# Performance work log

Measured on AMD Instinct MI355X. Metric: run time of the kernel, lower is better.

The kernel has to match this reference:

```python
import jax, jax.numpy as jnp
import numpy as np


def _build_space_group(L):
    # C4v point group: rotations R^k and mirror*R^k, acting on Z_L^2 coords.
    R = np.array([[0, -1], [1, 0]])
    Mr = np.array([[1, 0], [0, -1]])
    mats = [np.linalg.matrix_power(R, k) for k in range(4)]
    mats += [Mr @ m for m in mats[:4]]
    mats = np.array(mats)  # (8,2,2)
    P = 8

    def find(A):
        for i in range(P):
            if np.array_equal(mats[i], A):
                return i
        raise ValueError('point group not closed')

    pcomp = np.array([[find(mats[a] @ mats[b]) for b in range(P)] for a in range(P)])
    pinv = np.array([find(np.round(np.linalg.inv(mats[a])).astype(int)) for a in range(P)])

    N = L * L
    G = P * N
    gx, gy = np.meshgrid(np.arange(L), np.arange(L), indexing='ij')
    coords = np.stack([gx.ravel(), gy.ravel()], -1)  # (N,2): site coords, also translation vecs

    # element g = p*N + (tx*L+ty) acts on coord v as  M_p v + t  (mod L)
    perms = np.zeros((G, N), np.int64)
    for p in range(P):
        w = coords @ mats[p].T  # (N,2)
        for t in range(N):
            u = (w + coords[t]) % L
            perms[p * N + t] = u[:, 0] * L + u[:, 1]

    pa = np.repeat(np.arange(P), N)  # point part per element
    ta = np.tile(coords, (P, 1))     # translation part per element
    mult = np.zeros((G, G), np.int64)
    for g in range(G):
        Ma = mats[pa[g]]
        pprod = pcomp[pa[g], pa]            # (G,)
        tprod = (ta @ Ma.T + ta[g]) % L     # (G,2): M_a t_b + t_a
        mult[g] = pprod * N + tprod[:, 0] * L + tprod[:, 1]
    inv = np.zeros((G,), np.int64)
    for g in range(G):
        Mi = mats[pinv[pa[g]]]
        ti = (-(Mi @ ta[g])) % L            # -M^{-1} t
        inv[g] = pinv[pa[g]] * N + ti[0] * L + ti[1]
    return perms, mult, inv


L_SIDE = 8
FEATS = (8, 8, 8)
BATCH = 1024


def setup_inputs() -> dict:
    perms, mult, inv = _build_space_group(L_SIDE)
    N = L_SIDE * L_SIDE
    G = perms.shape[0]
    c0, c1, c2 = FEATS
    ks = jax.random.split(jax.random.key(0), 8)
    s = jax.random.normal(ks[0], (BATCH, N), jnp.float32)
    # lecun_normal: std = 1/sqrt(fan_in)
    W_lift = jax.random.normal(ks[1], (N, c0), jnp.float32) / np.sqrt(N)
    b_lift = jnp.zeros((c0,), jnp.float32)
    K0 = jax.random.normal(ks[2], (G, c0, c1), jnp.float32) / np.sqrt(G * c0)
    K1 = jax.random.normal(ks[3], (G, c1, c2), jnp.float32) / np.sqrt(G * c1)
    W_amp = jax.random.normal(ks[4], (c2, 1), jnp.float32) / np.sqrt(c2)
    b_amp = jnp.zeros((1,), jnp.float32)
    W_ph = jnp.zeros((c2, 1), jnp.float32)  # zeros init as in module
    b_ph = jnp.zeros((1,), jnp.float32)
    return {'s': s, 'perms': jnp.asarray(perms), 'mult': jnp.asarray(mult),
            'inv': jnp.asarray(inv), 'W_lift': W_lift, 'b_lift': b_lift,
            'K0': K0, 'K1': K1, 'W_amp': W_amp, 'b_amp': b_amp,
            'W_ph': W_ph, 'b_ph': b_ph}


def reference(s, perms, mult, inv, W_lift, b_lift, K0, K1, W_amp, b_amp, W_ph, b_ph):
    G = perms.shape[0]
    s_g = s[:, perms].astype(jnp.float32)          # (B,G,N): lift gather
    x = jax.nn.gelu(s_g @ W_lift + b_lift)         # (B,G,c0)
    T = mult[:, inv]                                # (G,G): T[g,h] = g * h^{-1}
    scale = 1.0 / jnp.sqrt(jnp.asarray(G, jnp.float32))
    for K in (K0, K1):
        Kg = K[T]                                   # (G,G,cin,cout) regular-rep kernel gather
        x = jax.nn.gelu(jnp.einsum('bhc,ghcd->bgd', x, Kg) * scale)
    pooled = jnp.mean(x, axis=1)                    # trivial irrep: chi = 1/G
    amp = (pooled @ W_amp + b_amp)[..., 0]          # (B,)
    phase = (pooled @ W_ph + b_ph)[..., 0]
    return (amp + 1j * phase).astype(jnp.complex64)
```

## Files before the change

kernel.cpp:

```cpp
#include <hip/hip_runtime.h>
#include <hip/hip_bf16.h>
#include <cstdint>
#include <cstddef>

using s16x8 = __attribute__((ext_vector_type(8))) short;
using u16x8 = __attribute__((ext_vector_type(8))) unsigned short;
using f32x4 = __attribute__((ext_vector_type(4))) float;

#define GC 4096
#define SCALE_G 0.04419417382415922f

__device__ __forceinline__ float gelu_f(float x) {
  float u = 0.7978845608028654f * (x + 0.044715f * x * x * x);
  return 0.5f * x * (1.0f + tanhf(u));
}

__device__ __forceinline__ unsigned short f2bf(float f) {
  unsigned int u = __float_as_uint(f);
  unsigned int r = (u + 0x7fffu + ((u >> 16) & 1u)) >> 16;
  return (unsigned short)r;
}
__device__ __forceinline__ float bf2f(unsigned short b) {
  return __uint_as_float(((unsigned int)b) << 16);
}

__device__ __forceinline__ int idx_stride(const int* __restrict__ identity_row) {
  return (identity_row[1] == 0 && identity_row[3] == 0 && identity_row[5] == 0) ? 2 : 1;
}

typedef __attribute__((address_space(1))) void gvoid;
typedef __attribute__((address_space(3))) void lvoid;
__device__ __forceinline__ void gld16(const void* g, void* l) {
  __builtin_amdgcn_global_load_lds((gvoid*)g, (lvoid*)l, 16, 0, 0);
}

__device__ __forceinline__ s16x8 gload16(const unsigned short* p) {
  s16x8 r;
  asm volatile("global_load_dwordx4 %0, %1, off" : "=v"(r) : "v"(p));
  return r;
}

__global__ __launch_bounds__(256) void k_prep(
    const float* __restrict__ s, const int* __restrict__ perms,
    const int* __restrict__ mult, const int* __restrict__ inv,
    const float* __restrict__ Wl, const float* __restrict__ K0,
    const float* __restrict__ K1,
    unsigned short* __restrict__ sb, unsigned short* __restrict__ WPT,
    unsigned int* __restrict__ TallP, unsigned short* __restrict__ K0T0,
    unsigned short* __restrict__ K0T1) {
  const int tid = blockIdx.x * 256 + threadIdx.x;
  if (tid < 65536) {
    sb[tid] = f2bf(s[tid]);
  } else if (tid < 98304) {
    const int st = idx_stride(perms);
    const int t2 = tid - 65536;
    const int n = t2 & 63, h = t2 >> 6;
    const int m = perms[(size_t)t2 * st];
#pragma unroll
    for (int c = 0; c < 8; ++c)
      WPT[(size_t)((h << 3) + c) * 64 + m] = f2bf(Wl[n * 8 + c]);
  } else if (tid < 229376) {
    const int st = idx_stride(mult);
    const int i3 = tid - 98304;
    const int g = i3 & 511, w = i3 >> 9;
    const int h0 = (w >> 2) * 8 + (w & 3), h1 = h0 + 4;
    const int ih0 = inv[(size_t)h0 * st], ih1 = inv[(size_t)h1 * st];
    const unsigned int tv0 = (unsigned int)mult[(size_t)((g << 9) + ih0) * st];
    const unsigned int tv1 = (unsigned int)mult[(size_t)((g << 9) + ih1) * st];
    TallP[(size_t)w * 512 + g] = tv0 | (tv1 << 16);
  } else if (tid < 262144) {
    const int t4 = tid - 229376;
    const int tgh = t4 >> 6, e = t4 & 63, d = e >> 3, c = e & 7;
    K0T0[tgh * 64 + d * 8 + c] = f2bf(K0[tgh * 64 + c * 8 + d]);
  } else if (tid < 294912) {
    const int t5 = tid - 262144;
    const int tgh = t5 >> 6, e = t5 & 63, d = e >> 3, c = e & 7;
    K0T1[tgh * 64 + d * 8 + c] = f2bf(K1[tgh * 64 + c * 8 + d]);
  }
}

__global__ __launch_bounds__(256) void gemm_bf16(
    const unsigned short* __restrict__ A,
    const unsigned short* __restrict__ BT,
    unsigned short* __restrict__ C,
    const float* __restrict__ bias8,
    float scale, int M, int N, int K) {
  constexpr int BM = 64, BN = 128, BK = 64;
  __shared__ __align__(16) unsigned short As[3][BM * BK];
  __shared__ __align__(16) unsigned short Bs[3][BN * BK];

  const int nbm = M / BM;
  int bid = blockIdx.x;
  {
    const int q = (nbm * (N / BN)) >> 3;
    bid = (bid & 7) * q + (bid >> 3);
  }
  const int bn = bid / nbm, bm = bid % nbm;

  const int t = threadIdx.x;
  const int wid = t >> 6, lane = t & 63;
  const int wm = (wid >> 1) << 5;
  const int wn = (wid & 1) << 6;
  const int lr = lane & 15, lq = lane >> 4;

  const unsigned short* gA[2];
  const unsigned short* gB[4];
#pragma unroll
  for (int is = 0; is < 2; ++is) {
    const int sidx = is * 256 + t, row = sidx >> 3, c = (sidx & 7) ^ (row & 7);
    gA[is] = A + (size_t)(bm * BM + row) * K + c * 8;
  }
#pragma unroll
  for (int is = 0; is < 4; ++is) {
    const int sidx = is * 256 + t, row = sidx >> 3, c = (sidx & 7) ^ (row & 7);
    gB[is] = BT + (size_t)(bn * BN + row) * K + c * 8;
  }

  int aoff[2][2], boff[4][2];
#pragma unroll
  for (int i = 0; i < 2; ++i) {
    const int row = wm + i * 16 + lr;
#pragma unroll
    for (int ks = 0; ks < 2; ++ks)
      aoff[i][ks] = (row * 8 + ((ks * 4 + lq) ^ (row & 7))) * 16;
  }
#pragma unroll
  for (int j = 0; j < 4; ++j) {
    const int row = wn + j * 16 + lr;
#pragma unroll
    for (int ks = 0; ks < 2; ++ks)
      boff[j][ks] = (row * 8 + ((ks * 4 + lq) ^ (row & 7))) * 16;
  }

  auto stage = [&](int kt, int buf) {
    const int koff = kt * BK;
    char* la = (char*)&As[buf][0];
    char* lb = (char*)&Bs[buf][0];
#pragma unroll
    for (int is = 0; is < 2; ++is) gld16(gA[is] + koff, la + (is * 256 + t) * 16);
#pragma unroll
    for (int is = 0; is < 4; ++is) gld16(gB[is] + koff, lb + (is * 256 + t) * 16);
  };

  f32x4 acc[2][4] = {};
  const int nt = K / BK;
  stage(0, 0);
  if (nt > 1) stage(1, 1);

  int cur = 0;
  for (int kt = 0; kt < nt; ++kt) {
    if (kt < nt - 1) asm volatile("s_waitcnt vmcnt(6)" ::: "memory");
    else             asm volatile("s_waitcnt vmcnt(0)" ::: "memory");
    __builtin_amdgcn_s_barrier();
    asm volatile("" ::: "memory");
    __builtin_amdgcn_sched_barrier(0);
    if (kt + 2 < nt) {
      int nb = cur + 2; if (nb >= 3) nb -= 3;
      stage(kt + 2, nb);
    }
    const char* Ac = (const char*)&As[cur][0];
    const char* Bc = (const char*)&Bs[cur][0];
#pragma unroll
    for (int ks = 0; ks < 2; ++ks) {
      s16x8 a0 = *(const s16x8*)(Ac + aoff[0][ks]);
      s16x8 a1 = *(const s16x8*)(Ac + aoff[1][ks]);
      s16x8 b0 = *(const s16x8*)(Bc + boff[0][ks]);
      s16x8 b1 = *(const s16x8*)(Bc + boff[1][ks]);
      s16x8 b2 = *(const s16x8*)(Bc + boff[2][ks]);
      s16x8 b3 = *(const s16x8*)(Bc + boff[3][ks]);
      acc[0][0] = __builtin_amdgcn_mfma_f32_16x16x32_bf16(a0, b0, acc[0][0], 0, 0, 0);
      acc[0][1] = __builtin_amdgcn_mfma_f32_16x16x32_bf16(a0, b1, acc[0][1], 0, 0, 0);
      acc[0][2] = __builtin_amdgcn_mfma_f32_16x16x32_bf16(a0, b2, acc[0][2], 0, 0, 0);
      acc[0][3] = __builtin_amdgcn_mfma_f32_16x16x32_bf16(a0, b3, acc[0][3], 0, 0, 0);
      acc[1][0] = __builtin_amdgcn_mfma_f32_16x16x32_bf16(a1, b0, acc[1][0], 0, 0, 0);
      acc[1][1] = __builtin_amdgcn_mfma_f32_16x16x32_bf16(a1, b1, acc[1][1], 0, 0, 0);
      acc[1][2] = __builtin_amdgcn_mfma_f32_16x16x32_bf16(a1, b2, acc[1][2], 0, 0, 0);
      acc[1][3] = __builtin_amdgcn_mfma_f32_16x16x32_bf16(a1, b3, acc[1][3], 0, 0, 0);
    }
    cur = (cur == 2) ? 0 : cur + 1;
  }

#pragma unroll
  for (int i = 0; i < 2; ++i) {
    const int row0 = bm * BM + wm + i * 16 + lq * 4;
#pragma unroll
    for (int j = 0; j < 4; ++j) {
      const int col = bn * BN + wn + j * 16 + lr;
      const float bv = bias8 ? bias8[col & 7] : 0.0f;
#pragma unroll
      for (int r = 0; r < 4; ++r) {
        float v = gelu_f(acc[i][j][r] * scale + bv);
        C[(size_t)(row0 + r) * N + col] = f2bf(v);
      }
    }
  }
}

template <int POOL>
__global__ __launch_bounds__(512, 2) void gemm_fused(
    const unsigned short* __restrict__ A,
    const unsigned short* __restrict__ K0T,
    const unsigned int* __restrict__ TallP,
    unsigned short* __restrict__ C,
    float* __restrict__ Ppart,
    float scale) {
  constexpr int Kdim = 4096, N = 4096, BM = 128, BK = 64, NT = Kdim / BK;
  __shared__ __align__(16) unsigned short As[3][BM * BK];
  __shared__ __align__(16) unsigned int TlP[64 * 4 * 16];

  const int bm = blockIdx.x & 7;
  const int bn = blockIdx.x >> 3;

  const int t = threadIdx.x;
  const int wid = t >> 6, lane = t & 63;
  const int wm = (wid >> 2) << 6;
  const int wn = (wid & 3) << 5;
  const int lr = lane & 15, lq = lane >> 4;
  const int glb = (wn >> 3) + (lr >> 3);
  const int dlo = lr & 7;

  const unsigned short* gA[2];
#pragma unroll
  for (int is = 0; is < 2; ++is) {
    const int sidx = is * 512 + t, row = sidx >> 3, c = (sidx & 7) ^ (row & 7);
    gA[is] = A + (size_t)(bm * BM + row) * Kdim + c * 8;
  }
  auto stage = [&](int kt, int buf) {
    const int koff = kt * BK;
    char* la = (char*)&As[buf][0];
#pragma unroll
    for (int is = 0; is < 2; ++is) gld16(gA[is] + koff, la + (is * 512 + t) * 16);
  };

  int aoff[4][2];
#pragma unroll
  for (int i = 0; i < 4; ++i) {
    const int row = wm + i * 16 + lr;
#pragma unroll
    for (int ks = 0; ks < 2; ++ks)
      aoff[i][ks] = (row * 8 + ((ks * 4 + lq) ^ (row & 7))) * 16;
  }

  stage(0, 0);
#pragma unroll
  for (int is = 0; is < 2; ++is) {
    const int sidx = is * 512 + t;
    const unsigned int* src =
        TallP + (size_t)(sidx >> 2) * 512 + bn * 16 + (sidx & 3) * 4;
    gld16(src, (char*)&TlP[0] + sidx * 16);
  }
  stage(1, 1);
  asm volatile("s_waitcnt vmcnt(0)" ::: "memory");
  __builtin_amdgcn_s_barrier();
  asm volatile("" ::: "memory");

  f32x4 acc[4][2] = {};
  s16x8 aA[4][2], aB[4][2];
  s16x8 bA[2][2], bB[2][2];
  unsigned int tvA[2], tvB[2];

  {
    unsigned int tv0[2];
#pragma unroll
    for (int j = 0; j < 2; ++j) tv0[j] = TlP[(0 * 4 + lq) * 16 + glb + j * 2];
#pragma unroll
    for (int j = 0; j < 2; ++j) tvA[j] = TlP[(1 * 4 + lq) * 16 + glb + j * 2];
#pragma unroll
    for (int j = 0; j < 2; ++j) {
      bA[j][0] = gload16(K0T + (tv0[j] & 0xFFFFu) * 64 + dlo * 8);
      bA[j][1] = gload16(K0T + (tv0[j] >> 16) * 64 + dlo * 8);
    }
    const char* Ac = (const char*)&As[0][0];
#pragma unroll
    for (int i = 0; i < 4; ++i)
#pragma unroll
      for (int ks = 0; ks < 2; ++ks)
        aA[i][ks] = *(const s16x8*)(Ac + aoff[i][ks]);
  }

  int cur = 0;
  auto iter = [&](int kt, s16x8 (&aC)[4][2], s16x8 (&aN)[4][2],
                  s16x8 (&bC)[2][2], s16x8 (&bN)[2][2],
                  unsigned int (&tvC)[2], unsigned int (&tvN)[2]) {
    asm volatile("s_waitcnt vmcnt(0)" ::: "memory");
    __builtin_amdgcn_s_barrier();
    asm volatile("" ::: "memory");
    int nxt = cur + 1; if (nxt >= 3) nxt -= 3;
    if (kt + 2 < NT) {
#pragma unroll
      for (int j = 0; j < 2; ++j)
        tvN[j] = TlP[((kt + 2) * 4 + lq) * 16 + glb + j * 2];
    }
    if (kt + 1 < NT) {
      const char* An = (const char*)&As[nxt][0];
#pragma unroll
      for (int i = 0; i < 4; ++i)
#pragma unroll
        for (int ks = 0; ks < 2; ++ks)
          aN[i][ks] = *(const s16x8*)(An + aoff[i][ks]);
#pragma unroll
      for (int j = 0; j < 2; ++j) {
        bN[j][0] = gload16(K0T + (tvC[j] & 0xFFFFu) * 64 + dlo * 8);
        bN[j][1] = gload16(K0T + (tvC[j] >> 16) * 64 + dlo * 8);
      }
      if (kt + 2 < NT) {
        int nb = cur + 2; if (nb >= 3) nb -= 3;
        stage(kt + 2, nb);
      }
    }
    __builtin_amdgcn_sched_barrier(0);
    __builtin_amdgcn_s_setprio(1);
#pragma unroll
    for (int ks = 0; ks < 2; ++ks)
#pragma unroll
      for (int i = 0; i < 4; ++i) {
        acc[i][0] = __builtin_amdgcn_mfma_f32_16x16x32_bf16(aC[i][ks], bC[0][ks],
                                                            acc[i][0], 0, 0, 0);
        acc[i][1] = __builtin_amdgcn_mfma_f32_16x16x32_bf16(aC[i][ks], bC[1][ks],
                                                            acc[i][1], 0, 0, 0);
      }
    __builtin_amdgcn_s_setprio(0);
    cur = nxt;
  };

  for (int kt2 = 0; kt2 < NT; kt2 += 2) {
    iter(kt2,     aA, aB, bA, bB, tvA, tvB);
    iter(kt2 + 1, aB, aA, bB, bA, tvB, tvA);
  }

  if (POOL == 0) {
#pragma unroll
    for (int i = 0; i < 4; ++i) {
      const int row0 = bm * BM + wm + i * 16 + lq * 4;
#pragma unroll
      for (int j = 0; j < 2; ++j) {
        const int col = bn * 128 + wn + j * 16 + lr;
#pragma unroll
        for (int r = 0; r < 4; ++r) {
          float v = gelu_f(acc[i][j][r] * scale);
          C[(size_t)(row0 + r) * N + col] = f2bf(v);
        }
      }
    }
  } else {
    const int plane = bn * 4 + (wn >> 5);
    float* Pp = Ppart + (size_t)plane * 8192;
#pragma unroll
    for (int i = 0; i < 4; ++i) {
      const int row0 = bm * BM + wm + i * 16 + lq * 4;
#pragma unroll
      for (int r = 0; r < 4; ++r) {
        float v = gelu_f(acc[i][0][r] * scale) + gelu_f(acc[i][1][r] * scale);
        v += __shfl_xor(v, 8);
        if (lr < 8) Pp[(row0 + r) * 8 + lr] = v * (1.0f / 512.0f);
      }
    }
  }
}

__global__ __launch_bounds__(256) void k_head(const float* __restrict__ Ppart,
                                              const float* __restrict__ Wamp,
                                              const float* __restrict__ bamp,
                                              const float* __restrict__ Wph,
                                              const float* __restrict__ bph,
                                              float* __restrict__ out,
                                              int out_size) {
  int b = blockIdx.x * 256 + threadIdx.x;
  if (b >= 1024) return;
  float acc8[8] = {};
  for (int p = 0; p < 128; ++p) {
    const float* src = Ppart + (size_t)p * 8192 + b * 8;
#pragma unroll
    for (int d = 0; d < 8; ++d) acc8[d] += src[d];
  }
  float a = bamp[0], ph = bph[0];
#pragma unroll
  for (int d = 0; d < 8; ++d) {
    a += acc8[d] * Wamp[d];
    ph += acc8[d] * Wph[d];
  }
  out[b] = a;
  if (out_size >= 2048) out[1024 + b] = ph;
}


extern "C" void kernel_launch(void* const* d_in, const int* in_sizes, int n_in,
                              void* d_out, int out_size, void* d_ws, size_t ws_size,
                              hipStream_t stream) {
  (void)in_sizes; (void)n_in; (void)ws_size;
  const float* s    = (const float*)d_in[0];
  const int*   perms= (const int*)d_in[1];
  const int*   mult = (const int*)d_in[2];
  const int*   inv  = (const int*)d_in[3];
  const float* Wl   = (const float*)d_in[4];
  const float* bl   = (const float*)d_in[5];
  const float* K0   = (const float*)d_in[6];
  const float* K1   = (const float*)d_in[7];
  const float* Wamp = (const float*)d_in[8];
  const float* bamp = (const float*)d_in[9];
  const float* Wph  = (const float*)d_in[10];
  const float* bph  = (const float*)d_in[11];
  float* out = (float*)d_out;

  char* ws = (char*)d_ws;
  unsigned short* X1  = (unsigned short*)(ws);
  unsigned short* X2  = (unsigned short*)(ws + (8u << 20));
  unsigned short* sb  = (unsigned short*)(ws + (16u << 20));
  unsigned short* WPT = (unsigned short*)(ws + (16u << 20) + (128u << 10));
  unsigned int*   TallP=(unsigned int*) (ws + (16u << 20) + (640u << 10));
  unsigned short* K0T0= (unsigned short*)(ws + (16u << 20) + (1152u << 10));
  unsigned short* K0T1= (unsigned short*)(ws + (16u << 20) + (1216u << 10));
  float* Ppart        = (float*)(ws + (18u << 20));

  k_prep<<<1152, 256, 0, stream>>>(s, perms, mult, inv, Wl, K0, K1,
                                   sb, WPT, TallP, K0T0, K0T1);
  gemm_bf16<<<512, 256, 0, stream>>>(sb, WPT, X1, bl, 1.0f, 1024, 4096, 64);
  gemm_fused<0><<<256, 512, 0, stream>>>(X1, K0T0, TallP, X2, nullptr, SCALE_G);
  gemm_fused<1><<<256, 512, 0, stream>>>(X2, K0T1, TallP, nullptr, Ppart, SCALE_G);
  k_head<<<4, 256, 0, stream>>>(Ppart, Wamp, bamp, Wph, bph, out, out_size);
}
```

Measured before the change: 132.1 us.

## Deepen fused-GEMM A prefetch to three stages and parallelize head reduction

The fused GEMM now issues A-tile loads three iterations ahead instead of two, reusing the just-consumed LDS buffer. It waits with a partial vmcnt so only the oldest stage must land before the barrier, which should hide more global latency. The pooled partials are stored batch-major, so the head kernel runs one block per batch row and reduces the 128 planes in LDS instead of 4 blocks looping serially. The risks are a race if vmcnt(2) does not match the actual count of outstanding loads (the B gathers are also global loads), and overwriting buffer 'cur' while other waves may still be reading it.

```diff
diff --git a/kernel.cpp b/kernel.cpp
--- a/kernel.cpp
+++ b/kernel.cpp
@@ -242,6 +242,7 @@
   }
 
   stage(0, 0);
+  stage(1, 1);
 #pragma unroll
   for (int is = 0; is < 2; ++is) {
     const int sidx = is * 512 + t;
@@ -249,7 +250,6 @@
         TallP + (size_t)(sidx >> 2) * 512 + bn * 16 + (sidx & 3) * 4;
     gld16(src, (char*)&TlP[0] + sidx * 16);
   }
-  stage(1, 1);
   asm volatile("s_waitcnt vmcnt(0)" ::: "memory");
   __builtin_amdgcn_s_barrier();
   asm volatile("" ::: "memory");
@@ -270,6 +270,7 @@
       bA[j][0] = gload16(K0T + (tv0[j] & 0xFFFFu) * 64 + dlo * 8);
       bA[j][1] = gload16(K0T + (tv0[j] >> 16) * 64 + dlo * 8);
     }
+    stage(2, 2);
     const char* Ac = (const char*)&As[0][0];
 #pragma unroll
     for (int i = 0; i < 4; ++i)
@@ -282,7 +283,8 @@
   auto iter = [&](int kt, s16x8 (&aC)[4][2], s16x8 (&aN)[4][2],
                   s16x8 (&bC)[2][2], s16x8 (&bN)[2][2],
                   unsigned int (&tvC)[2], unsigned int (&tvN)[2]) {
-    asm volatile("s_waitcnt vmcnt(0)" ::: "memory");
+    if (kt < NT - 2) asm volatile("s_waitcnt vmcnt(2)" ::: "memory");
+    else             asm volatile("s_waitcnt vmcnt(0)" ::: "memory");
     __builtin_amdgcn_s_barrier();
     asm volatile("" ::: "memory");
     int nxt = cur + 1; if (nxt >= 3) nxt -= 3;
@@ -303,11 +305,8 @@
         bN[j][0] = gload16(K0T + (tvC[j] & 0xFFFFu) * 64 + dlo * 8);
         bN[j][1] = gload16(K0T + (tvC[j] >> 16) * 64 + dlo * 8);
       }
-      if (kt + 2 < NT) {
-        int nb = cur + 2; if (nb >= 3) nb -= 3;
-        stage(kt + 2, nb);
-      }
-    }
+    }
+    if (kt + 3 < NT) stage(kt + 3, cur);
     __builtin_amdgcn_sched_barrier(0);
     __builtin_amdgcn_s_setprio(1);
 #pragma unroll
@@ -344,7 +343,6 @@
     }
   } else {
     const int plane = bn * 4 + (wn >> 5);
-    float* Pp = Ppart + (size_t)plane * 8192;
 #pragma unroll
     for (int i = 0; i < 4; ++i) {
       const int row0 = bm * BM + wm + i * 16 + lq * 4;
@@ -352,35 +350,45 @@
       for (int r = 0; r < 4; ++r) {
         float v = gelu_f(acc[i][0][r] * scale) + gelu_f(acc[i][1][r] * scale);
         v += __shfl_xor(v, 8);
-        if (lr < 8) Pp[(row0 + r) * 8 + lr] = v * (1.0f / 512.0f);
+        if (lr < 8)
+          Ppart[((size_t)(row0 + r) * 128 + plane) * 8 + lr] = v * (1.0f / 512.0f);
       }
     }
   }
 }
 
-__global__ __launch_bounds__(256) void k_head(const float* __restrict__ Ppart,
+__global__ __launch_bounds__(128) void k_head(const float* __restrict__ Ppart,
                                               const float* __restrict__ Wamp,
                                               const float* __restrict__ bamp,
                                               const float* __restrict__ Wph,
                                               const float* __restrict__ bph,
                                               float* __restrict__ out,
                                               int out_size) {
-  int b = blockIdx.x * 256 + threadIdx.x;
-  if (b >= 1024) return;
-  float acc8[8] = {};
-  for (int p = 0; p < 128; ++p) {
-    const float* src = Ppart + (size_t)p * 8192 + b * 8;
-#pragma unroll
-    for (int d = 0; d < 8; ++d) acc8[d] += src[d];
-  }
-  float a = bamp[0], ph = bph[0];
-#pragma unroll
-  for (int d = 0; d < 8; ++d) {
-    a += acc8[d] * Wamp[d];
-    ph += acc8[d] * Wph[d];
-  }
-  out[b] = a;
-  if (out_size >= 2048) out[1024 + b] = ph;
+  __shared__ float red[128 * 8 + 8];
+  const int b = blockIdx.x, t = threadIdx.x;
+  const float* src = Ppart + ((size_t)b * 128 + t) * 8;
+  f32x4 v0 = *(const f32x4*)(src);
+  f32x4 v1 = *(const f32x4*)(src + 4);
+  *(f32x4*)(red + t * 8) = v0;
+  *(f32x4*)(red + t * 8 + 4) = v1;
+  __syncthreads();
+  if (t < 8) {
+    float s = 0.f;
+#pragma unroll 16
+    for (int p = 0; p < 128; ++p) s += red[p * 8 + t];
+    red[1024 + t] = s;
+  }
+  __syncthreads();
+  if (t == 0) {
+    float a = bamp[0], ph = bph[0];
+#pragma unroll
+    for (int d = 0; d < 8; ++d) {
+      a += red[1024 + d] * Wamp[d];
+      ph += red[1024 + d] * Wph[d];
+    }
+    out[b] = a;
+    if (out_size >= 2048) out[1024 + b] = ph;
+  }
 }
 
 
@@ -417,5 +425,5 @@
   gemm_bf16<<<512, 256, 0, stream>>>(sb, WPT, X1, bl, 1.0f, 1024, 4096, 64);
   gemm_fused<0><<<256, 512, 0, stream>>>(X1, K0T0, TallP, X2, nullptr, SCALE_G);
   gemm_fused<1><<<256, 512, 0, stream>>>(X2, K0T1, TallP, nullptr, Ppart, SCALE_G);
-  k_head<<<4, 256, 0, stream>>>(Ppart, Wamp, bamp, Wph, bph, out, out_size);
-}
+  k_head<<<1024, 128, 0, stream>>>(Ppart, Wamp, bamp, Wph, bph, out, out_size);
+}
```

Result: faster. 110.5 us (-16.3%).
